# Kernel tuning notes

Hardware: AMD Instinct MI355X
Metric: run time of the kernel (lower is better)

## Reference

```python
import jax, jax.numpy as jnp
import numpy as np

LAMBDA = 0.95   # fast-weight decay
ETA = 0.5       # Hebbian write rate
EPS = 1e-5      # LayerNorm epsilon
S_LOOP = 2      # inner read steps


def setup_inputs() -> dict:
    key = jax.random.key(0)
    ks = jax.random.split(key, 3)
    T, B, d_g, d_h = 32, 32, 256, 512
    z_seq = jax.random.normal(ks[0], (T, B, d_g), dtype=jnp.float32)
    # kaiming-uniform-ish / xavier-ish scaled weights
    W_h = jax.random.normal(ks[1], (d_h, d_h), dtype=jnp.float32) * (2.0 / d_h) ** 0.5
    W_g = jax.random.normal(ks[2], (d_h, d_g), dtype=jnp.float32) * (2.0 / (d_h + d_g)) ** 0.5
    b_h = jnp.zeros((d_h,), jnp.float32)
    ln_gamma = jnp.ones((d_h,), jnp.float32)
    ln_beta = jnp.zeros((d_h,), jnp.float32)
    return {"z_seq": z_seq, "W_h": W_h, "W_g": W_g, "b_h": b_h,
            "ln_gamma": ln_gamma, "ln_beta": ln_beta}


def reference(z_seq, W_h, W_g, b_h, ln_gamma, ln_beta):
    T, B, _ = z_seq.shape
    d_h = W_h.shape[0]

    def ln(x):
        mu = jnp.mean(x, axis=-1, keepdims=True)
        var = jnp.mean((x - mu) ** 2, axis=-1, keepdims=True)
        return (x - mu) * jax.lax.rsqrt(var + EPS) * ln_gamma + ln_beta

    def inner_read(h_base, A):
        # h = relu(LN(h_base)); then S fast-weight reads h <- relu(LN(h_base + A h))
        h = jax.nn.relu(ln(h_base))
        for _ in range(S_LOOP):
            Ah = jnp.einsum('bij,bj->bi', A, h)  # [B, d_h]
            h = jax.nn.relu(ln(h_base + Ah))
        return h

    def step(carry, z_t):
        h, A = carry
        h_base = h @ W_h.T + z_t @ W_g.T + b_h  # [B, d_h]
        h = inner_read(h_base, A)
        # Hebbian outer-product write: A <- lambda*A + eta * h h^T
        A = LAMBDA * A + ETA * jnp.einsum('bi,bj->bij', h, h)
        return (h, A), None

    h0 = jnp.zeros((B, d_h), z_seq.dtype)
    A0 = jnp.zeros((B, d_h, d_h), z_seq.dtype)
    (h, A), _ = jax.lax.scan(step, (h0, A0), z_seq[:-1])

    # last step: read-only (no A update)
    h_base = h @ W_h.T + z_seq[-1] @ W_g.T + b_h
    h = inner_read(h_base, A)
    return h
```

## Files before the change

kernel.cpp:

```cpp
#include <hip/hip_runtime.h>

typedef __attribute__((ext_vector_type(8))) short short8;
typedef __attribute__((ext_vector_type(4))) float f32x4;

constexpr int T_STEPS = 32;
constexpr int BATCH   = 32;
constexpr int DG      = 256;
constexpr int DH      = 512;
constexpr int NHIST   = 31;
constexpr int LDA     = 608;
constexpr float LAMBDA_ = 0.95f;
constexpr float ETA_    = 0.5f;
constexpr float EPS_    = 1e-5f;

__device__ __forceinline__ uint bf16cvt(float f) {
  uint u = __float_as_uint(f);
  return (u + 0x7FFFu + ((u >> 16) & 1u)) >> 16;
}
__device__ __forceinline__ uint pack2(float a, float b) {
  return bf16cvt(a) | (bf16cvt(b) << 16);
}

__global__ __launch_bounds__(512) void pack_kernel(
    const float* __restrict__ Wh, uint4* __restrict__ Wp) {
  const int f  = blockIdx.x * 512 + threadIdx.x;
  const int lf = f & 63;
  const int kk = (f >> 6) & 15;
  const int mt = f >> 10;
  const int r  = mt * 16 + (lf & 15);
  const int k0 = kk * 32 + (lf >> 4) * 8;
  const float4 a = *reinterpret_cast<const float4*>(Wh + (size_t)r * DH + k0);
  const float4 b = *reinterpret_cast<const float4*>(Wh + (size_t)r * DH + k0 + 4);
  Wp[f] = make_uint4(pack2(a.x, a.y), pack2(a.z, a.w),
                     pack2(b.x, b.y), pack2(b.z, b.w));
}

__global__ __launch_bounds__(512, 2) void rnn_kernel(
    const uint4* __restrict__ Wp, const float* __restrict__ z,
    const float* __restrict__ Wg, const float* __restrict__ bh,
    const float* __restrict__ g, const float* __restrict__ be,
    float* __restrict__ out) {
  __shared__ float  area[T_STEPS * LDA];
  __shared__ float  part[DH];
  __shared__ float  h_s[DH];
  __shared__ ushort hbf[DH];
  __shared__ float  red1[8], red2[8];
  __shared__ float  cc[NHIST + 1];
  __shared__ float  lam_pow[NHIST];

  const int tid  = threadIdx.x;
  const int lane = tid & 63;
  const int wave = tid >> 6;
  const int c    = lane & 15;
  const int gq   = lane >> 4;
  const int b    = blockIdx.x;
  const int r    = tid;

  if (tid == 0) {
    float p = 1.f;
    for (int k = 0; k < NHIST; ++k) { lam_pow[k] = p; p *= LAMBDA_; }
  }

#pragma unroll
  for (int mt4 = 0; mt4 < 4; ++mt4) {
    const int mt = wave * 4 + mt4;
    f32x4 acc0 = {0.f,0.f,0.f,0.f}, acc1 = {0.f,0.f,0.f,0.f};
#pragma unroll
    for (int kk = 0; kk < 8; ++kk) {
      const int k0 = kk * 32 + gq * 8;
      const float4 a  = *reinterpret_cast<const float4*>(Wg + (size_t)(mt*16 + c) * DG + k0);
      const float4 a2 = *reinterpret_cast<const float4*>(Wg + (size_t)(mt*16 + c) * DG + k0 + 4);
      const uint4 afu = make_uint4(pack2(a.x,a.y), pack2(a.z,a.w),
                                   pack2(a2.x,a2.y), pack2(a2.z,a2.w));
      const float* zb0 = z + ((size_t)c        * BATCH + b) * DG + k0;
      const float* zb1 = z + ((size_t)(16 + c) * BATCH + b) * DG + k0;
      const float4 b00 = *reinterpret_cast<const float4*>(zb0);
      const float4 b01 = *reinterpret_cast<const float4*>(zb0 + 4);
      const float4 b10 = *reinterpret_cast<const float4*>(zb1);
      const float4 b11 = *reinterpret_cast<const float4*>(zb1 + 4);
      const uint4 bf0 = make_uint4(pack2(b00.x,b00.y), pack2(b00.z,b00.w),
                                   pack2(b01.x,b01.y), pack2(b01.z,b01.w));
      const uint4 bf1 = make_uint4(pack2(b10.x,b10.y), pack2(b10.z,b10.w),
                                   pack2(b11.x,b11.y), pack2(b11.z,b11.w));
      acc0 = __builtin_amdgcn_mfma_f32_16x16x32_bf16(
          __builtin_bit_cast(short8, afu), __builtin_bit_cast(short8, bf0), acc0, 0,0,0);
      acc1 = __builtin_amdgcn_mfma_f32_16x16x32_bf16(
          __builtin_bit_cast(short8, afu), __builtin_bit_cast(short8, bf1), acc1, 0,0,0);
    }
    *reinterpret_cast<f32x4*>(&area[(size_t)c        * LDA + mt*16 + gq*4]) = acc0;
    *reinterpret_cast<f32x4*>(&area[(size_t)(16 + c) * LDA + mt*16 + gq*4]) = acc1;
  }
  __syncthreads();

  const float bh_r = bh[r], g_r = g[r], be_r = be[r];

  auto ln = [&](float x) -> float {
    float s1 = x, s2 = x * x;
#pragma unroll
    for (int off = 32; off; off >>= 1) {
      s1 += __shfl_xor(s1, off, 64);
      s2 += __shfl_xor(s2, off, 64);
    }
    if (lane == 0) { red1[wave] = s1; red2[wave] = s2; }
    __syncthreads();
    float a = 0.f, q = 0.f;
#pragma unroll
    for (int w2 = 0; w2 < 8; ++w2) { a += red1[w2]; q += red2[w2]; }
    const float mu = a * (1.f / DH);
    const float rs = rsqrtf(q * (1.f / DH) - mu * mu + EPS_);
    const float hv2 = fmaxf((x - mu) * rs * g_r + be_r, 0.f);
    h_s[r] = hv2;
    hbf[r] = (ushort)bf16cvt(hv2);
    __syncthreads();
    return hv2;
  };

  float hv = 0.f;
  for (int t = 0; t < T_STEPS; ++t) {
    float xb;
    if (t == 0) {
      xb = area[r] + bh_r;
    } else {
      f32x4 acc[4] = {{0.f,0.f,0.f,0.f},{0.f,0.f,0.f,0.f},
                      {0.f,0.f,0.f,0.f},{0.f,0.f,0.f,0.f}};
#pragma unroll
      for (int kk = 0; kk < 16; ++kk) {
        uint4 bvu = {0u,0u,0u,0u};
        if (c == 0)
          bvu = *reinterpret_cast<const uint4*>(&hbf[kk*32 + gq*8]);
        const short8 bv = __builtin_bit_cast(short8, bvu);
#pragma unroll
        for (int mt4 = 0; mt4 < 4; ++mt4) {
          const int mt = wave * 4 + mt4;
          const uint4 au = Wp[(size_t)(mt*16 + kk) * 64 + lane];
          acc[mt4] = __builtin_amdgcn_mfma_f32_16x16x32_bf16(
              __builtin_bit_cast(short8, au), bv, acc[mt4], 0,0,0);
        }
      }
      if (c == 0) {
#pragma unroll
        for (int mt4 = 0; mt4 < 4; ++mt4)
          *reinterpret_cast<f32x4*>(&part[(wave*4 + mt4)*16 + gq*4]) = acc[mt4];
      }
      __syncthreads();
      xb = part[r] + area[(size_t)t * LDA + r] + bh_r;
    }

    hv = ln(xb);

    if (t > 0) {
      for (int s = 0; s < 2; ++s) {
        const float4 c0 = *reinterpret_cast<const float4*>(&h_s[lane * 8]);
        const float4 c1 = *reinterpret_cast<const float4*>(&h_s[lane * 8 + 4]);
        for (int sp = wave; sp < t; sp += 8) {
          const float* hr = &area[(size_t)sp * LDA];
          const float4 a0 = *reinterpret_cast<const float4*>(&hr[lane * 8]);
          const float4 a1 = *reinterpret_cast<const float4*>(&hr[lane * 8 + 4]);
          float d = c0.x*a0.x + c0.y*a0.y + c0.z*a0.z + c0.w*a0.w
                  + c1.x*a1.x + c1.y*a1.y + c1.z*a1.z + c1.w*a1.w;
#pragma unroll
          for (int off = 32; off; off >>= 1) d += __shfl_xor(d, off, 64);
          if (lane == 0) cc[sp] = ETA_ * lam_pow[t - 1 - sp] * d;
        }
        __syncthreads();
        float ah = 0.f;
        for (int sp = 0; sp < t; ++sp) ah = fmaf(cc[sp], area[(size_t)sp * LDA + r], ah);
        hv = ln(xb + ah);
      }
    }

    if (t < T_STEPS - 1) area[(size_t)t * LDA + r] = hv;
  }

  out[(size_t)b * DH + r] = hv;
}

extern "C" void kernel_launch(void* const* d_in, const int* in_sizes, int n_in,
                              void* d_out, int out_size, void* d_ws, size_t ws_size,
                              hipStream_t stream) {
  const float* z     = (const float*)d_in[0];
  const float* W_h   = (const float*)d_in[1];
  const float* W_g   = (const float*)d_in[2];
  const float* b_h   = (const float*)d_in[3];
  const float* gamma = (const float*)d_in[4];
  const float* beta  = (const float*)d_in[5];
  float* out = (float*)d_out;

  uint4* Wp = (uint4*)d_ws;

  pack_kernel<<<dim3(64), dim3(512), 0, stream>>>(W_h, Wp);
  rnn_kernel<<<dim3(BATCH), dim3(512), 0, stream>>>(Wp, z, W_g, b_h,
                                                    gamma, beta, out);
}
```

Measured before the change: 306.0 us.

## Keep half of W_h fragments in registers and store transposed bf16 history

Half of each wave's W_h MFMA fragments (8 of 16 k-slices) are preloaded into registers once, so the per-step recurrent matmul reloads only the other half from global memory. A transposed bf16 copy of the hidden-state history is kept in shared memory, letting each thread read its row's history with four 128-bit loads in a fixed unrolled loop instead of t strided fp32 loads. This unrolled loop always covers 32 history slots and relies on cc being zeroed for unused entries. The costs are more register pressure (128 extra VGPRs) that may hurt occupancy or cause spills, and reduced precision in the A·h read because the history is stored in bf16.

Result: faster. 292.4 us (-4.5%).

```diff
diff --git a/kernel.cpp b/kernel.cpp
--- a/kernel.cpp
+++ b/kernel.cpp
@@ -8,7 +8,8 @@
 constexpr int DG      = 256;
 constexpr int DH      = 512;
 constexpr int NHIST   = 31;
-constexpr int LDA     = 608;
+constexpr int LDA     = 544;
+constexpr int LDT     = 40;
 constexpr float LAMBDA_ = 0.95f;
 constexpr float ETA_    = 0.5f;
 constexpr float EPS_    = 1e-5f;
@@ -19,6 +20,9 @@
 }
 __device__ __forceinline__ uint pack2(float a, float b) {
   return bf16cvt(a) | (bf16cvt(b) << 16);
+}
+__device__ __forceinline__ float bf2f(ushort u) {
+  return __uint_as_float(((uint)u) << 16);
 }
 
 __global__ __launch_bounds__(512) void pack_kernel(
@@ -41,6 +45,7 @@
     const float* __restrict__ g, const float* __restrict__ be,
     float* __restrict__ out) {
   __shared__ float  area[T_STEPS * LDA];
+  __shared__ ushort histT[DH][LDT];
   __shared__ float  part[DH];
   __shared__ float  h_s[DH];
   __shared__ ushort hbf[DH];
@@ -60,6 +65,14 @@
     float p = 1.f;
     for (int k = 0; k < NHIST; ++k) { lam_pow[k] = p; p *= LAMBDA_; }
   }
+  if (tid < NHIST + 1) cc[tid] = 0.f;
+
+  uint4 wfr[4][8];
+#pragma unroll
+  for (int mt4 = 0; mt4 < 4; ++mt4)
+#pragma unroll
+    for (int kk = 0; kk < 8; ++kk)
+      wfr[mt4][kk] = Wp[(size_t)((wave * 4 + mt4) * 16 + kk) * 64 + lane];
 
 #pragma unroll
   for (int mt4 = 0; mt4 < 4; ++mt4) {
@@ -124,15 +137,25 @@
       f32x4 acc[4] = {{0.f,0.f,0.f,0.f},{0.f,0.f,0.f,0.f},
                       {0.f,0.f,0.f,0.f},{0.f,0.f,0.f,0.f}};
 #pragma unroll
-      for (int kk = 0; kk < 16; ++kk) {
+      for (int kk = 0; kk < 8; ++kk) {
         uint4 bvu = {0u,0u,0u,0u};
         if (c == 0)
           bvu = *reinterpret_cast<const uint4*>(&hbf[kk*32 + gq*8]);
         const short8 bv = __builtin_bit_cast(short8, bvu);
 #pragma unroll
+        for (int mt4 = 0; mt4 < 4; ++mt4)
+          acc[mt4] = __builtin_amdgcn_mfma_f32_16x16x32_bf16(
+              __builtin_bit_cast(short8, wfr[mt4][kk]), bv, acc[mt4], 0,0,0);
+      }
+#pragma unroll
+      for (int kk = 8; kk < 16; ++kk) {
+        uint4 bvu = {0u,0u,0u,0u};
+        if (c == 0)
+          bvu = *reinterpret_cast<const uint4*>(&hbf[kk*32 + gq*8]);
+        const short8 bv = __builtin_bit_cast(short8, bvu);
+#pragma unroll
         for (int mt4 = 0; mt4 < 4; ++mt4) {
-          const int mt = wave * 4 + mt4;
-          const uint4 au = Wp[(size_t)(mt*16 + kk) * 64 + lane];
+          const uint4 au = Wp[(size_t)((wave*4 + mt4)*16 + kk) * 64 + lane];
           acc[mt4] = __builtin_amdgcn_mfma_f32_16x16x32_bf16(
               __builtin_bit_cast(short8, au), bv, acc[mt4], 0,0,0);
         }
@@ -164,12 +187,27 @@
         }
         __syncthreads();
         float ah = 0.f;
-        for (int sp = 0; sp < t; ++sp) ah = fmaf(cc[sp], area[(size_t)sp * LDA + r], ah);
+#pragma unroll
+        for (int q8 = 0; q8 < 4; ++q8) {
+          const uint4 hw = *reinterpret_cast<const uint4*>(&histT[r][q8 * 8]);
+          const uint w0 = hw.x, w1 = hw.y, w2 = hw.z, w3 = hw.w;
+          ah = fmaf(cc[q8*8+0], __uint_as_float(w0 << 16),          ah);
+          ah = fmaf(cc[q8*8+1], __uint_as_float(w0 & 0xFFFF0000u),  ah);
+          ah = fmaf(cc[q8*8+2], __uint_as_float(w1 << 16),          ah);
+          ah = fmaf(cc[q8*8+3], __uint_as_float(w1 & 0xFFFF0000u),  ah);
+          ah = fmaf(cc[q8*8+4], __uint_as_float(w2 << 16),          ah);
+          ah = fmaf(cc[q8*8+5], __uint_as_float(w2 & 0xFFFF0000u),  ah);
+          ah = fmaf(cc[q8*8+6], __uint_as_float(w3 << 16),          ah);
+          ah = fmaf(cc[q8*8+7], __uint_as_float(w3 & 0xFFFF0000u),  ah);
+        }
         hv = ln(xb + ah);
       }
     }
 
-    if (t < T_STEPS - 1) area[(size_t)t * LDA + r] = hv;
+    if (t < T_STEPS - 1) {
+      area[(size_t)t * LDA + r] = hv;
+      histT[r][t] = (ushort)bf16cvt(hv);
+    }
   }
 
   out[(size_t)b * DH + r] = hv;
```
